# Kernel tuning notes

Hardware: AMD Instinct MI355X
Metric: run time of the kernel (lower is better)

Reference implementation:

```python
import jax, jax.numpy as jnp
import numpy as np

N, E, IN_DIM, HID, OUT = 50000, 600000, 128, 256, 128

def setup_inputs() -> dict:
    key = jax.random.key(0)
    k1, k2, k3, k4, k5, k6, k7 = jax.random.split(key, 7)
    h = jax.random.normal(k1, (N, IN_DIM), dtype=jnp.float32)
    src = jax.random.randint(k2, (E,), 0, N)
    dst = jax.random.randint(k3, (E,), 0, N)
    s1 = 1.0 / np.sqrt(2 * IN_DIM)
    s2 = 1.0 / np.sqrt(HID)
    W1 = jax.random.uniform(k4, (2 * IN_DIM, HID), minval=-s1, maxval=s1, dtype=jnp.float32)
    b1 = jax.random.uniform(k5, (HID,), minval=-s1, maxval=s1, dtype=jnp.float32)
    W2 = jax.random.uniform(k6, (HID, OUT), minval=-s2, maxval=s2, dtype=jnp.float32)
    b2 = jax.random.uniform(k7, (OUT,), minval=-s2, maxval=s2, dtype=jnp.float32)
    return {"h": h, "src": src, "dst": dst, "W1": W1, "b1": b1, "W2": W2, "b2": b2}

def reference(h, src, dst, W1, b1, W2, b2):
    n = h.shape[0]
    # copy_u + mean: gather src features, segment-sum at dst, divide by in-degree
    msg_sum = jax.ops.segment_sum(h[src], dst, num_segments=n)          # [N, D]
    deg = jax.ops.segment_sum(jnp.ones((src.shape[0],), h.dtype), dst, num_segments=n)
    h_neigh = msg_sum / jnp.maximum(deg, 1.0)[:, None]                  # zero-deg nodes -> 0
    h_total = jnp.concatenate([h, h_neigh], axis=1)                     # [N, 2D]
    out = (h_total @ W1 + b1) @ W2 + b2                                 # 2-layer MLP (no inner activation)
    return jax.nn.relu(out)
```

## Files before the change

kernel.cpp:

```cpp
#include <hip/hip_runtime.h>

#define N_NODES 50000
#define E_EDGES 600000
#define IN_DIM  128
#define HID     256
#define OUT_DIM 128
#define CAP     64

#define NB_FILL 2344
#define NB_HCVT 6250
#define NB_WCVT 384

typedef __bf16 bf16x8 __attribute__((ext_vector_type(8)));
typedef float  f32x16 __attribute__((ext_vector_type(16)));

__device__ __forceinline__ unsigned short f2bf(float f) {
    union { float f; unsigned int i; } v; v.f = f;
    unsigned int b = v.i;
    b += 0x7fffu + ((b >> 16) & 1u);
    return (unsigned short)(b >> 16);
}
__device__ __forceinline__ float bf2f(unsigned short u) {
    union { unsigned int i; float f; } v; v.i = ((unsigned int)u) << 16; return v.f;
}

__global__ void __launch_bounds__(256)
sage_prep(const int* __restrict__ src, const int* __restrict__ dst,
          int* __restrict__ counts, int* __restrict__ bucket,
          const float* __restrict__ h, unsigned short* __restrict__ ht,
          const float* __restrict__ W1, const float* __restrict__ W2,
          unsigned short* __restrict__ w1sw, unsigned short* __restrict__ w2sw) {
    int b = blockIdx.x;
    if (b < NB_FILL) {
        int e = b * 256 + threadIdx.x;
        if (e < E_EDGES) {
            int d = dst[e];
            int slot = atomicAdd(counts + d, 1);
            if (slot < CAP) bucket[(size_t)d * CAP + slot] = src[e];
        }
    } else if (b < NB_FILL + NB_HCVT) {
        int idx = (b - NB_FILL) * 256 + threadIdx.x;
        if (idx < N_NODES * 32) {
            int n = idx >> 5, g = idx & 31;
            const float4 v = *(const float4*)(h + (size_t)n * IN_DIM + g * 4);
            ushort4 o;
            o.x = f2bf(v.x); o.y = f2bf(v.y); o.z = f2bf(v.z); o.w = f2bf(v.w);
            *(ushort4*)(ht + (size_t)n * 256 + g * 4) = o;
        }
    } else {
        int i = (b - NB_FILL - NB_HCVT) * 256 + threadIdx.x;
        if (i < 65536) {
            int j = i & 7, n = (i >> 3) & 255, g = (i >> 11) & 1, ks = (i >> 12) & 3, c = i >> 14;
            int k = c * 64 + ks * 16 + g * 8 + j;
            w1sw[i] = f2bf(W1[(size_t)k * HID + n]);
        } else {
            int i2 = i - 65536;
            int j = i2 & 7, n = (i2 >> 3) & 127, g = (i2 >> 10) & 1, ks = (i2 >> 11) & 7, c = (i2 >> 14) & 1;
            int k = c * 128 + ks * 16 + g * 8 + j;
            w2sw[i2] = f2bf(W2[(size_t)k * OUT_DIM + n]);
        }
    }
}

__global__ void __launch_bounds__(256)
sage_gather(const int* __restrict__ counts,
            const int* __restrict__ bucket,
            unsigned short* ht) {
    int node = blockIdx.x * 8 + (threadIdx.x >> 5);
    int l = threadIdx.x & 31;
    if (node >= N_NODES) return;

    int dg = counts[node];
    int entries = min(dg, CAP);
    const int* bk = bucket + (size_t)node * CAP;

    float a0 = 0.f, a1 = 0.f, a2 = 0.f, a3 = 0.f;
    int e = 0;
    for (; e + 4 <= entries; e += 4) {
        const int4 s = *(const int4*)(bk + e);
        const ushort4 v0 = *(const ushort4*)(ht + (size_t)s.x * 256 + l * 4);
        const ushort4 v1 = *(const ushort4*)(ht + (size_t)s.y * 256 + l * 4);
        const ushort4 v2 = *(const ushort4*)(ht + (size_t)s.z * 256 + l * 4);
        const ushort4 v3 = *(const ushort4*)(ht + (size_t)s.w * 256 + l * 4);
        a0 += bf2f(v0.x) + bf2f(v1.x) + bf2f(v2.x) + bf2f(v3.x);
        a1 += bf2f(v0.y) + bf2f(v1.y) + bf2f(v2.y) + bf2f(v3.y);
        a2 += bf2f(v0.z) + bf2f(v1.z) + bf2f(v2.z) + bf2f(v3.z);
        a3 += bf2f(v0.w) + bf2f(v1.w) + bf2f(v2.w) + bf2f(v3.w);
    }
    for (; e < entries; ++e) {
        const ushort4 v = *(const ushort4*)(ht + (size_t)bk[e] * 256 + l * 4);
        a0 += bf2f(v.x); a1 += bf2f(v.y); a2 += bf2f(v.z); a3 += bf2f(v.w);
    }
    float inv = 1.0f / (float)max(dg, 1);
    ushort4 o;
    o.x = f2bf(a0 * inv); o.y = f2bf(a1 * inv);
    o.z = f2bf(a2 * inv); o.w = f2bf(a3 * inv);
    *(ushort4*)(ht + (size_t)node * 256 + 128 + l * 4) = o;
}

__global__ void __launch_bounds__(256)
sage_mlp(const unsigned short* ht,
         const unsigned short* __restrict__ w1sw,
         const unsigned short* __restrict__ w2sw,
         const float* __restrict__ b1,
         const float* __restrict__ b2,
         float* out) {
    __shared__ unsigned short wbuf[16384];
    __shared__ unsigned short hid_s[64][264];

    const int t = threadIdx.x;
    const int nw = t >> 6;
    const int lane = t & 63;
    const int lr = lane & 31;
    const int lg = lane >> 5;
    const int base = blockIdx.x * 64;
    const int row0 = min(base + lr,      N_NODES - 1);
    const int row1 = min(base + 32 + lr, N_NODES - 1);

    f32x16 c1[2][2];
    #pragma unroll
    for (int e = 0; e < 16; ++e) {
        c1[0][0][e] = 0.f; c1[0][1][e] = 0.f; c1[1][0][e] = 0.f; c1[1][1][e] = 0.f;
    }

    #pragma unroll
    for (int c = 0; c < 4; ++c) {
        if (c) __syncthreads();
        {
            const bf16x8* gsrc = (const bf16x8*)(w1sw + c * 16384);
            #pragma unroll
            for (int i = 0; i < 8; ++i) {
                int off16 = i * 256 + t;
                *(bf16x8*)(wbuf + off16 * 8) = gsrc[off16];
            }
        }
        bf16x8 a0[4], a1[4];
        #pragma unroll
        for (int ks = 0; ks < 4; ++ks) {
            int koff = (c * 4 + ks) * 16 + lg * 8;
            a0[ks] = *(const bf16x8*)(ht + (size_t)row0 * 256 + koff);
            a1[ks] = *(const bf16x8*)(ht + (size_t)row1 * 256 + koff);
        }
        __syncthreads();
        #pragma unroll
        for (int ks = 0; ks < 4; ++ks) {
            #pragma unroll
            for (int nt = 0; nt < 2; ++nt) {
                int n = nw * 64 + nt * 32 + lr;
                bf16x8 b = *(const bf16x8*)(wbuf + (((ks * 2 + lg) * 256) + n) * 8);
                c1[0][nt] = __builtin_amdgcn_mfma_f32_32x32x16_bf16(a0[ks], b, c1[0][nt], 0, 0, 0);
                c1[1][nt] = __builtin_amdgcn_mfma_f32_32x32x16_bf16(a1[ks], b, c1[1][nt], 0, 0, 0);
            }
        }
    }

    #pragma unroll
    for (int nt = 0; nt < 2; ++nt) {
        int col = nw * 64 + nt * 32 + lr;
        float bias = b1[col];
        #pragma unroll
        for (int s = 0; s < 2; ++s) {
            #pragma unroll
            for (int reg = 0; reg < 16; ++reg) {
                int m = s * 32 + (reg & 3) + 8 * (reg >> 2) + 4 * lg;
                hid_s[m][col] = f2bf(c1[s][nt][reg] + bias);
            }
        }
    }
    __syncthreads();

    f32x16 c2[2];
    #pragma unroll
    for (int e = 0; e < 16; ++e) { c2[0][e] = 0.f; c2[1][e] = 0.f; }

    #pragma unroll
    for (int c = 0; c < 2; ++c) {
        if (c) __syncthreads();
        {
            const bf16x8* gsrc = (const bf16x8*)(w2sw + c * 16384);
            #pragma unroll
            for (int i = 0; i < 8; ++i) {
                int off16 = i * 256 + t;
                *(bf16x8*)(wbuf + off16 * 8) = gsrc[off16];
            }
        }
        __syncthreads();
        #pragma unroll
        for (int ks = 0; ks < 8; ++ks) {
            bf16x8 b = *(const bf16x8*)(wbuf + ((ks * 2 + lg) * 128 + nw * 32 + lr) * 8);
            int koff = c * 128 + ks * 16 + lg * 8;
            bf16x8 ah0 = *(const bf16x8*)(&hid_s[lr][koff]);
            bf16x8 ah1 = *(const bf16x8*)(&hid_s[32 + lr][koff]);
            c2[0] = __builtin_amdgcn_mfma_f32_32x32x16_bf16(ah0, b, c2[0], 0, 0, 0);
            c2[1] = __builtin_amdgcn_mfma_f32_32x32x16_bf16(ah1, b, c2[1], 0, 0, 0);
        }
    }

    {
        int col = nw * 32 + lr;
        float bias = b2[col];
        #pragma unroll
        for (int s = 0; s < 2; ++s) {
            #pragma unroll
            for (int reg = 0; reg < 16; ++reg) {
                int m = s * 32 + (reg & 3) + 8 * (reg >> 2) + 4 * lg;
                int n = base + m;
                if (n < N_NODES)
                    out[(size_t)n * OUT_DIM + col] = fmaxf(c2[s][reg] + bias, 0.0f);
            }
        }
    }
}

extern "C" void kernel_launch(void* const* d_in, const int* in_sizes, int n_in,
                              void* d_out, int out_size, void* d_ws, size_t ws_size,
                              hipStream_t stream) {
    const float* h   = (const float*)d_in[0];
    const int*   src = (const int*)d_in[1];
    const int*   dst = (const int*)d_in[2];
    const float* W1  = (const float*)d_in[3];
    const float* b1  = (const float*)d_in[4];
    const float* W2  = (const float*)d_in[5];
    const float* b2  = (const float*)d_in[6];
    float* out = (float*)d_out;

    unsigned short* ht = (unsigned short*)d_out;

    int* counts = (int*)d_ws;
    int* bucket = counts + N_NODES;
    unsigned short* w1sw = (unsigned short*)(bucket + (size_t)N_NODES * CAP);
    unsigned short* w2sw = w1sw + 65536;

    hipMemsetAsync(counts, 0, N_NODES * sizeof(int), stream);

    sage_prep<<<NB_FILL + NB_HCVT + NB_WCVT, 256, 0, stream>>>(
        src, dst, counts, bucket, h, ht, W1, W2, w1sw, w2sw);

    sage_gather<<<(N_NODES + 7) / 8, 256, 0, stream>>>(counts, bucket, ht);

    sage_mlp<<<(N_NODES + 63) / 64, 256, 0, stream>>>(ht, w1sw, w2sw, b1, b2, out);
}
```

Baseline: 182.9 us.

## Fuse neighbor-mean gather into MLP kernel with shared-memory mean tile

```diff
diff --git a/kernel.cpp b/kernel.cpp
--- a/kernel.cpp
+++ b/kernel.cpp
@@ -8,11 +8,12 @@
 #define CAP     64
 
 #define NB_FILL 2344
-#define NB_HCVT 6250
+#define NB_HCVT 3125
 #define NB_WCVT 384
 
 typedef __bf16 bf16x8 __attribute__((ext_vector_type(8)));
 typedef float  f32x16 __attribute__((ext_vector_type(16)));
+typedef unsigned short u16x8 __attribute__((ext_vector_type(8)));
 
 __device__ __forceinline__ unsigned short f2bf(float f) {
     union { float f; unsigned int i; } v; v.f = f;
@@ -40,73 +41,41 @@
         }
     } else if (b < NB_FILL + NB_HCVT) {
         int idx = (b - NB_FILL) * 256 + threadIdx.x;
-        if (idx < N_NODES * 32) {
-            int n = idx >> 5, g = idx & 31;
-            const float4 v = *(const float4*)(h + (size_t)n * IN_DIM + g * 4);
-            ushort4 o;
-            o.x = f2bf(v.x); o.y = f2bf(v.y); o.z = f2bf(v.z); o.w = f2bf(v.w);
-            *(ushort4*)(ht + (size_t)n * 256 + g * 4) = o;
-        }
+        int n = idx >> 4, g = idx & 15;
+        const float4 v0 = *(const float4*)(h + (size_t)n * IN_DIM + g * 8);
+        const float4 v1 = *(const float4*)(h + (size_t)n * IN_DIM + g * 8 + 4);
+        u16x8 o;
+        o[0] = f2bf(v0.x); o[1] = f2bf(v0.y); o[2] = f2bf(v0.z); o[3] = f2bf(v0.w);
+        o[4] = f2bf(v1.x); o[5] = f2bf(v1.y); o[6] = f2bf(v1.z); o[7] = f2bf(v1.w);
+        *(u16x8*)(ht + (size_t)n * IN_DIM + g * 8) = o;
     } else {
         int i = (b - NB_FILL - NB_HCVT) * 256 + threadIdx.x;
         if (i < 65536) {
-            int j = i & 7, n = (i >> 3) & 255, g = (i >> 11) & 1, ks = (i >> 12) & 3, c = i >> 14;
-            int k = c * 64 + ks * 16 + g * 8 + j;
+            int j = i & 7, n = (i >> 3) & 255, k16 = i >> 11;
+            int k = (k16 >> 1) * 16 + (k16 & 1) * 8 + j;
             w1sw[i] = f2bf(W1[(size_t)k * HID + n]);
         } else {
             int i2 = i - 65536;
-            int j = i2 & 7, n = (i2 >> 3) & 127, g = (i2 >> 10) & 1, ks = (i2 >> 11) & 7, c = (i2 >> 14) & 1;
-            int k = c * 128 + ks * 16 + g * 8 + j;
+            int j = i2 & 7, n = (i2 >> 3) & 127, k16 = i2 >> 10;
+            int k = (k16 >> 1) * 16 + (k16 & 1) * 8 + j;
             w2sw[i2] = f2bf(W2[(size_t)k * OUT_DIM + n]);
         }
     }
 }
 
 __global__ void __launch_bounds__(256)
-sage_gather(const int* __restrict__ counts,
-            const int* __restrict__ bucket,
-            unsigned short* ht) {
-    int node = blockIdx.x * 8 + (threadIdx.x >> 5);
-    int l = threadIdx.x & 31;
-    if (node >= N_NODES) return;
-
-    int dg = counts[node];
-    int entries = min(dg, CAP);
-    const int* bk = bucket + (size_t)node * CAP;
-
-    float a0 = 0.f, a1 = 0.f, a2 = 0.f, a3 = 0.f;
-    int e = 0;
-    for (; e + 4 <= entries; e += 4) {
-        const int4 s = *(const int4*)(bk + e);
-        const ushort4 v0 = *(const ushort4*)(ht + (size_t)s.x * 256 + l * 4);
-        const ushort4 v1 = *(const ushort4*)(ht + (size_t)s.y * 256 + l * 4);
-        const ushort4 v2 = *(const ushort4*)(ht + (size_t)s.z * 256 + l * 4);
-        const ushort4 v3 = *(const ushort4*)(ht + (size_t)s.w * 256 + l * 4);
-        a0 += bf2f(v0.x) + bf2f(v1.x) + bf2f(v2.x) + bf2f(v3.x);
-        a1 += bf2f(v0.y) + bf2f(v1.y) + bf2f(v2.y) + bf2f(v3.y);
-        a2 += bf2f(v0.z) + bf2f(v1.z) + bf2f(v2.z) + bf2f(v3.z);
-        a3 += bf2f(v0.w) + bf2f(v1.w) + bf2f(v2.w) + bf2f(v3.w);
-    }
-    for (; e < entries; ++e) {
-        const ushort4 v = *(const ushort4*)(ht + (size_t)bk[e] * 256 + l * 4);
-        a0 += bf2f(v.x); a1 += bf2f(v.y); a2 += bf2f(v.z); a3 += bf2f(v.w);
-    }
-    float inv = 1.0f / (float)max(dg, 1);
-    ushort4 o;
-    o.x = f2bf(a0 * inv); o.y = f2bf(a1 * inv);
-    o.z = f2bf(a2 * inv); o.w = f2bf(a3 * inv);
-    *(ushort4*)(ht + (size_t)node * 256 + 128 + l * 4) = o;
-}
-
-__global__ void __launch_bounds__(256)
-sage_mlp(const unsigned short* ht,
+sage_mlp(const unsigned short* __restrict__ ht,
+         const int* __restrict__ counts,
+         const int* __restrict__ bucket,
          const unsigned short* __restrict__ w1sw,
          const unsigned short* __restrict__ w2sw,
          const float* __restrict__ b1,
          const float* __restrict__ b2,
-         float* out) {
-    __shared__ unsigned short wbuf[16384];
-    __shared__ unsigned short hid_s[64][264];
+         float* __restrict__ out) {
+    __shared__ unsigned short wbuf[8192];
+    __shared__ unsigned short pool[16896];
+    unsigned short* mean_s = pool;
+    unsigned short* hid_s  = pool;
 
     const int t = threadIdx.x;
     const int nw = t >> 6;
@@ -117,80 +86,137 @@
     const int row0 = min(base + lr,      N_NODES - 1);
     const int row1 = min(base + 32 + lr, N_NODES - 1);
 
+    #pragma unroll
+    for (int mi = 0; mi < 8; ++mi) {
+        int m = nw * 16 + lg * 8 + mi;
+        int node = base + m;
+        float a0 = 0.f, a1 = 0.f, a2 = 0.f, a3 = 0.f;
+        int dg = 0;
+        if (node < N_NODES) {
+            dg = counts[node];
+            int en = min(dg, CAP);
+            const int* bk = bucket + (size_t)node * CAP;
+            int e = 0;
+            for (; e + 8 <= en; e += 8) {
+                const int4 sA = *(const int4*)(bk + e);
+                const int4 sB = *(const int4*)(bk + e + 4);
+                const ushort4 v0 = *(const ushort4*)(ht + (size_t)sA.x * IN_DIM + lr * 4);
+                const ushort4 v1 = *(const ushort4*)(ht + (size_t)sA.y * IN_DIM + lr * 4);
+                const ushort4 v2 = *(const ushort4*)(ht + (size_t)sA.z * IN_DIM + lr * 4);
+                const ushort4 v3 = *(const ushort4*)(ht + (size_t)sA.w * IN_DIM + lr * 4);
+                const ushort4 v4 = *(const ushort4*)(ht + (size_t)sB.x * IN_DIM + lr * 4);
+                const ushort4 v5 = *(const ushort4*)(ht + (size_t)sB.y * IN_DIM + lr * 4);
+                const ushort4 v6 = *(const ushort4*)(ht + (size_t)sB.z * IN_DIM + lr * 4);
+                const ushort4 v7 = *(const ushort4*)(ht + (size_t)sB.w * IN_DIM + lr * 4);
+                a0 += bf2f(v0.x)+bf2f(v1.x)+bf2f(v2.x)+bf2f(v3.x)+bf2f(v4.x)+bf2f(v5.x)+bf2f(v6.x)+bf2f(v7.x);
+                a1 += bf2f(v0.y)+bf2f(v1.y)+bf2f(v2.y)+bf2f(v3.y)+bf2f(v4.y)+bf2f(v5.y)+bf2f(v6.y)+bf2f(v7.y);
+                a2 += bf2f(v0.z)+bf2f(v1.z)+bf2f(v2.z)+bf2f(v3.z)+bf2f(v4.z)+bf2f(v5.z)+bf2f(v6.z)+bf2f(v7.z);
+                a3 += bf2f(v0.w)+bf2f(v1.w)+bf2f(v2.w)+bf2f(v3.w)+bf2f(v4.w)+bf2f(v5.w)+bf2f(v6.w)+bf2f(v7.w);
+            }
+            if (e + 4 <= en) {
+                const int4 sA = *(const int4*)(bk + e);
+                const ushort4 v0 = *(const ushort4*)(ht + (size_t)sA.x * IN_DIM + lr * 4);
+                const ushort4 v1 = *(const ushort4*)(ht + (size_t)sA.y * IN_DIM + lr * 4);
+                const ushort4 v2 = *(const ushort4*)(ht + (size_t)sA.z * IN_DIM + lr * 4);
+                const ushort4 v3 = *(const ushort4*)(ht + (size_t)sA.w * IN_DIM + lr * 4);
+                a0 += bf2f(v0.x)+bf2f(v1.x)+bf2f(v2.x)+bf2f(v3.x);
+                a1 += bf2f(v0.y)+bf2f(v1.y)+bf2f(v2.y)+bf2f(v3.y);
+                a2 += bf2f(v0.z)+bf2f(v1.z)+bf2f(v2.z)+bf2f(v3.z);
+                a3 += bf2f(v0.w)+bf2f(v1.w)+bf2f(v2.w)+bf2f(v3.w);
+                e += 4;
+            }
+            for (; e < en; ++e) {
+                const ushort4 v = *(const ushort4*)(ht + (size_t)bk[e] * IN_DIM + lr * 4);
+                a0 += bf2f(v.x); a1 += bf2f(v.y); a2 += bf2f(v.z); a3 += bf2f(v.w);
+            }
+        }
+        float inv = 1.0f / (float)max(dg, 1);
+        ushort4 o;
+        o.x = f2bf(a0 * inv); o.y = f2bf(a1 * inv);
+        o.z = f2bf(a2 * inv); o.w = f2bf(a3 * inv);
+        *(ushort4*)(mean_s + m * 132 + lr * 4) = o;
+    }
+
     f32x16 c1[2][2];
     #pragma unroll
     for (int e = 0; e < 16; ++e) {
         c1[0][0][e] = 0.f; c1[0][1][e] = 0.f; c1[1][0][e] = 0.f; c1[1][1][e] = 0.f;
     }
+
+    #pragma unroll
+    for (int c = 0; c < 8; ++c) {
+        if (c) __syncthreads();
+        {
+            const bf16x8* gsrc = (const bf16x8*)(w1sw + c * 8192);
+            #pragma unroll
+            for (int i = 0; i < 4; ++i) {
+                int off16 = i * 256 + t;
+                *(bf16x8*)(wbuf + off16 * 8) = gsrc[off16];
+            }
+        }
+        bf16x8 a0[2], a1[2];
+        #pragma unroll
+        for (int ks = 0; ks < 2; ++ks) {
+            int koff = c * 32 + ks * 16 + lg * 8;
+            if (c < 4) {
+                a0[ks] = *(const bf16x8*)(ht + (size_t)row0 * IN_DIM + koff);
+                a1[ks] = *(const bf16x8*)(ht + (size_t)row1 * IN_DIM + koff);
+            } else {
+                a0[ks] = *(const bf16x8*)(mean_s + lr * 132 + (koff - 128));
+                a1[ks] = *(const bf16x8*)(mean_s + (32 + lr) * 132 + (koff - 128));
+            }
+        }
+        __syncthreads();
+        #pragma unroll
+        for (int ks = 0; ks < 2; ++ks) {
+            #pragma unroll
+            for (int nt = 0; nt < 2; ++nt) {
+                int n = nw * 64 + nt * 32 + lr;
+                bf16x8 b = *(const bf16x8*)(wbuf + ((ks * 2 + lg) * 256 + n) * 8);
+                c1[0][nt] = __builtin_amdgcn_mfma_f32_32x32x16_bf16(a0[ks], b, c1[0][nt], 0, 0, 0);
+                c1[1][nt] = __builtin_amdgcn_mfma_f32_32x32x16_bf16(a1[ks], b, c1[1][nt], 0, 0, 0);
+            }
+        }
+    }
+    __syncthreads();
+
+    #pragma unroll
+    for (int nt = 0; nt < 2; ++nt) {
+        int col = nw * 64 + nt * 32 + lr;
+        float bias = b1[col];
+        #pragma unroll
+        for (int s = 0; s < 2; ++s) {
+            #pragma unroll
+            for (int reg = 0; reg < 16; ++reg) {
+                int m = s * 32 + (reg & 3) + 8 * (reg >> 2) + 4 * lg;
+                hid_s[m * 264 + col] = f2bf(c1[s][nt][reg] + bias);
+            }
+        }
+    }
+    __syncthreads();
+
+    f32x16 c2[2];
+    #pragma unroll
+    for (int e = 0; e < 16; ++e) { c2[0][e] = 0.f; c2[1][e] = 0.f; }
 
     #pragma unroll
     for (int c = 0; c < 4; ++c) {
         if (c) __syncthreads();
         {
-            const bf16x8* gsrc = (const bf16x8*)(w1sw + c * 16384);
-            #pragma unroll
-            for (int i = 0; i < 8; ++i) {
+            const bf16x8* gsrc = (const bf16x8*)(w2sw + c * 8192);
+            #pragma unroll
+            for (int i = 0; i < 4; ++i) {
                 int off16 = i * 256 + t;
                 *(bf16x8*)(wbuf + off16 * 8) = gsrc[off16];
             }
         }
-        bf16x8 a0[4], a1[4];
+        __syncthreads();
         #pragma unroll
         for (int ks = 0; ks < 4; ++ks) {
-            int koff = (c * 4 + ks) * 16 + lg * 8;
-            a0[ks] = *(const bf16x8*)(ht + (size_t)row0 * 256 + koff);
-            a1[ks] = *(const bf16x8*)(ht + (size_t)row1 * 256 + koff);
-        }
-        __syncthreads();
-        #pragma unroll
-        for (int ks = 0; ks < 4; ++ks) {
-            #pragma unroll
-            for (int nt = 0; nt < 2; ++nt) {
-                int n = nw * 64 + nt * 32 + lr;
-                bf16x8 b = *(const bf16x8*)(wbuf + (((ks * 2 + lg) * 256) + n) * 8);
-                c1[0][nt] = __builtin_amdgcn_mfma_f32_32x32x16_bf16(a0[ks], b, c1[0][nt], 0, 0, 0);
-                c1[1][nt] = __builtin_amdgcn_mfma_f32_32x32x16_bf16(a1[ks], b, c1[1][nt], 0, 0, 0);
-            }
-        }
-    }
-
-    #pragma unroll
-    for (int nt = 0; nt < 2; ++nt) {
-        int col = nw * 64 + nt * 32 + lr;
-        float bias = b1[col];
-        #pragma unroll
-        for (int s = 0; s < 2; ++s) {
-            #pragma unroll
-            for (int reg = 0; reg < 16; ++reg) {
-                int m = s * 32 + (reg & 3) + 8 * (reg >> 2) + 4 * lg;
-                hid_s[m][col] = f2bf(c1[s][nt][reg] + bias);
-            }
-        }
-    }
-    __syncthreads();
-
-    f32x16 c2[2];
-    #pragma unroll
-    for (int e = 0; e < 16; ++e) { c2[0][e] = 0.f; c2[1][e] = 0.f; }
-
-    #pragma unroll
-    for (int c = 0; c < 2; ++c) {
-        if (c) __syncthreads();
-        {
-            const bf16x8* gsrc = (const bf16x8*)(w2sw + c * 16384);
-            #pragma unroll
-            for (int i = 0; i < 8; ++i) {
-                int off16 = i * 256 + t;
-                *(bf16x8*)(wbuf + off16 * 8) = gsrc[off16];
-            }
-        }
-        __syncthreads();
-        #pragma unroll
-        for (int ks = 0; ks < 8; ++ks) {
             bf16x8 b = *(const bf16x8*)(wbuf + ((ks * 2 + lg) * 128 + nw * 32 + lr) * 8);
-            int koff = c * 128 + ks * 16 + lg * 8;
-            bf16x8 ah0 = *(const bf16x8*)(&hid_s[lr][koff]);
-            bf16x8 ah1 = *(const bf16x8*)(&hid_s[32 + lr][koff]);
+            int koff = c * 64 + ks * 16 + lg * 8;
+            bf16x8 ah0 = *(const bf16x8*)(hid_s + lr * 264 + koff);
+            bf16x8 ah1 = *(const bf16x8*)(hid_s + (32 + lr) * 264 + koff);
             c2[0] = __builtin_amdgcn_mfma_f32_32x32x16_bf16(ah0, b, c2[0], 0, 0, 0);
             c2[1] = __builtin_amdgcn_mfma_f32_32x32x16_bf16(ah1, b, c2[1], 0, 0, 0);
         }
@@ -224,19 +250,17 @@
     const float* b2  = (const float*)d_in[6];
     float* out = (float*)d_out;
 
-    unsigned short* ht = (unsigned short*)d_out;
-
     int* counts = (int*)d_ws;
     int* bucket = counts + N_NODES;
     unsigned short* w1sw = (unsigned short*)(bucket + (size_t)N_NODES * CAP);
     unsigned short* w2sw = w1sw + 65536;
+    unsigned short* ht   = w2sw + 32768;
 
     hipMemsetAsync(counts, 0, N_NODES * sizeof(int), stream);
 
     sage_prep<<<NB_FILL + NB_HCVT + NB_WCVT, 256, 0, stream>>>(
         src, dst, counts, bucket, h, ht, W1, W2, w1sw, w2sw);
 
-    sage_gather<<<(N_NODES + 7) / 8, 256, 0, stream>>>(counts, bucket, ht);
-
-    sage_mlp<<<(N_NODES + 63) / 64, 256, 0, stream>>>(ht, w1sw, w2sw, b1, b2, out);
-}
+    sage_mlp<<<(N_NODES + 63) / 64, 256, 0, stream>>>(
+        ht, counts, bucket, w1sw, w2sw, b1, b2, out);
+}
```

Result: slower. 219.5 us (+20.0%).
